# Optimization experiments

Hardware: AMD Instinct MI355X
Metric: run time of the kernel (lower is better)

## Reference

```python
import jax, jax.numpy as jnp
import numpy as np

TOPK_FRAC = 0.05
TOPK_MIN = 5
TOPK_MAX = 64


def setup_inputs() -> dict:
    key = jax.random.key(0)
    ks = jax.random.split(key, 8)
    N, H, B = 131072, 256, 512
    x = jax.random.normal(ks[0], (N, H), dtype=jnp.float32)
    batch = jnp.sort(jax.random.randint(ks[1], (N,), 0, B, dtype=jnp.int32))
    W1 = jax.random.normal(ks[2], (H, H // 2), dtype=jnp.float32) * 0.05
    b1 = jax.random.normal(ks[3], (H // 2,), dtype=jnp.float32) * 0.05
    W2 = jax.random.normal(ks[4], (H // 2, 1), dtype=jnp.float32) * 0.05
    b2 = jax.random.normal(ks[5], (1,), dtype=jnp.float32) * 0.05
    Wf = jax.random.normal(ks[6], (4 * H, H), dtype=jnp.float32) * 0.05
    bf = jax.random.normal(ks[7], (H,), dtype=jnp.float32) * 0.05
    return {"x": x, "batch": batch, "W1": W1, "b1": b1, "W2": W2,
            "b2": b2, "Wf": Wf, "bf": bf, "num_graphs": B}


def _forward(x, batch, W1, b1, W2, b2, Wf, bf, B):
    N = x.shape[0]
    # attention scores per node: MLP -> scalar
    s = (jax.nn.relu(x @ W1 + b1) @ W2 + b2)[:, 0]  # [N]
    # pyg_softmax: segment-wise stable softmax over nodes of each graph
    seg_max = jax.ops.segment_max(s, batch, num_segments=B)
    seg_max = jnp.where(jnp.isfinite(seg_max), seg_max, 0.0)  # guard empty segs
    e = jnp.exp(s - seg_max[batch])
    denom = jax.ops.segment_sum(e, batch, num_segments=B)
    w = e / denom[batch]                                    # [N]
    # pools
    x_attn = jax.ops.segment_sum(x * w[:, None], batch, num_segments=B)
    counts = jax.ops.segment_sum(jnp.ones((N,), jnp.int32), batch, num_segments=B)
    cnt_f = jnp.maximum(counts, 1).astype(x.dtype)
    x_mean = jax.ops.segment_sum(x, batch, num_segments=B) / cnt_f[:, None]
    x_max = jax.ops.segment_max(x, batch, num_segments=B)
    x_max = jnp.where(counts[:, None] > 0, x_max, 0.0)
    # per-graph dynamic k
    n = counts
    k = jnp.maximum(TOPK_MIN, jnp.ceil(TOPK_FRAC * n.astype(jnp.float32)).astype(jnp.int32))
    k = jnp.minimum(jnp.minimum(k, TOPK_MAX), n)            # [B]
    # fused segment top-k mean: sort nodes by (batch asc, w desc), keep rank<k
    order = jnp.lexsort((-w, batch))
    starts = jnp.concatenate([jnp.zeros((1,), jnp.int32), jnp.cumsum(counts)[:-1].astype(jnp.int32)])
    bs = batch[order]
    rank = jnp.arange(N, dtype=jnp.int32) - starts[bs]
    sel = (rank < k[bs]).astype(x.dtype)
    x_topk = jax.ops.segment_sum(x[order] * sel[:, None], bs, num_segments=B)
    x_topk = x_topk / jnp.maximum(k, 1).astype(x.dtype)[:, None]
    g = jax.nn.relu(jnp.concatenate([x_mean, x_attn, x_max, x_topk], axis=1) @ Wf + bf)
    return g


def reference(x, batch, W1, b1, W2, b2, Wf, bf, num_graphs):
    return _forward(x, batch, W1, b1, W2, b2, Wf, bf, num_graphs)
```

## Files before the change

### kernel.cpp

```cpp
#include <hip/hip_runtime.h>
#include <math.h>

#define H 256
#define HH 128
#define B_GRAPHS 512

typedef __attribute__((ext_vector_type(8))) short bfrag8;
typedef __attribute__((ext_vector_type(16))) float f32x16;

__global__ void k_prep_w1(const float* __restrict__ W1, ushort* __restrict__ W1b) {
  const int idx = blockIdx.x * 256 + threadIdx.x;
  const int k = idx >> 7, c = idx & 127;
  const float v = W1[idx];
  const uint u = __builtin_bit_cast(uint, v);
  const float r = v - __builtin_bit_cast(float, u & 0xFFFF0000u);
  const int base = (((k >> 4) * 2 + ((k >> 3) & 1)) * 128 + c) * 8 + (k & 7);
  W1b[base] = (ushort)(u >> 16);
  W1b[32768 + base] = (ushort)(__builtin_bit_cast(uint, r) >> 16);
}

__global__ void k_seg_bounds(const int* __restrict__ batch, int* __restrict__ seg_start,
                             int N, int B) {
  int b = blockIdx.x * blockDim.x + threadIdx.x;
  if (b > B) return;
  int lo = 0, hi = N;
  while (lo < hi) {
    int mid = (lo + hi) >> 1;
    if (batch[mid] < b) lo = mid + 1; else hi = mid;
  }
  seg_start[b] = lo;
}

__global__ __launch_bounds__(256, 4) void k_score_mfma(
    const float* __restrict__ x, const ushort* __restrict__ W1b,
    const float* __restrict__ b1, const float* __restrict__ W2,
    const float* __restrict__ b2, float* __restrict__ s_out) {
  __shared__ ushort ash[2][32][260];
  const int t = threadIdx.x;
  const int lane = t & 63;
  const int w = t >> 6;
  const int nl = lane & 31, g = lane >> 5;
  const int node0 = blockIdx.x * 32;

  {
    const float* base = x + (size_t)node0 * H + w * 2048 + lane * 4;
    float4 v[8];
#pragma unroll
    for (int i = 0; i < 8; ++i) v[i] = *(const float4*)(base + i * 256);
#pragma unroll
    for (int i = 0; i < 8; ++i) {
      const int r = w * 8 + i;
      const float vals[4] = {v[i].x, v[i].y, v[i].z, v[i].w};
      ushort m[4], rr[4];
#pragma unroll
      for (int e = 0; e < 4; ++e) {
        const uint u = __builtin_bit_cast(uint, vals[e]);
        m[e] = (ushort)(u >> 16);
        const float res = vals[e] - __builtin_bit_cast(float, u & 0xFFFF0000u);
        rr[e] = (ushort)(__builtin_bit_cast(uint, res) >> 16);
      }
      *(uint2*)&ash[0][r][lane * 4] =
          make_uint2((uint)m[0] | ((uint)m[1] << 16), (uint)m[2] | ((uint)m[3] << 16));
      *(uint2*)&ash[1][r][lane * 4] =
          make_uint2((uint)rr[0] | ((uint)rr[1] << 16), (uint)rr[2] | ((uint)rr[3] << 16));
    }
  }
  __syncthreads();

  f32x16 acc[2];
  acc[0] = (f32x16)0.f;
  acc[1] = (f32x16)0.f;
  const ushort* bbase = W1b + (size_t)(w * 32 + nl) * 8 + (size_t)g * 1024;

#pragma unroll
  for (int kks = 0; kks < 16; ++kks) {
    const bfrag8 a0 = *(const bfrag8*)&ash[0][nl][kks * 16 + g * 8];
    const bfrag8 a1 = *(const bfrag8*)&ash[1][nl][kks * 16 + g * 8];
    const bfrag8 b0 = *(const bfrag8*)(bbase + kks * 2048);
    const bfrag8 b1f = *(const bfrag8*)(bbase + kks * 2048 + 32768);
    acc[0] = __builtin_amdgcn_mfma_f32_32x32x16_bf16(a0, b0, acc[0], 0, 0, 0);
    acc[1] = __builtin_amdgcn_mfma_f32_32x32x16_bf16(a0, b1f, acc[1], 0, 0, 0);
    acc[0] = __builtin_amdgcn_mfma_f32_32x32x16_bf16(a1, b0, acc[0], 0, 0, 0);
  }

  __syncthreads();
  float* part = (float*)ash;
#pragma unroll
  for (int r = 0; r < 16; ++r) {
    const int row = (r & 3) + 8 * (r >> 2) + 4 * g;
    part[row * 132 + w * 32 + nl] = acc[0][r] + acc[1][r];
  }
  __syncthreads();
  {
    const int node = t >> 3, seg = t & 7;
    float v = 0.f;
#pragma unroll
    for (int e = 0; e < 16; ++e) {
      const int hcol = seg * 16 + e;
      const float hv = part[node * 132 + hcol] + b1[hcol];
      v = fmaf(fmaxf(hv, 0.f), W2[hcol], v);
    }
#pragma unroll
    for (int m = 1; m <= 4; m <<= 1) v += __shfl_xor(v, m);
    if ((t & 7) == 0) s_out[node0 + node] = v + b2[0];
  }
}

__global__ __launch_bounds__(512) void k_pool_fused(const float* __restrict__ x,
                                                    const float* __restrict__ s,
                                                    const int* __restrict__ seg_start,
                                                    float* __restrict__ pooled) {
  const int b = blockIdx.x;
  const int t = threadIdx.x;
  const int start = seg_start[b];
  const int end = seg_start[b + 1];
  const int n = end - start;

  __shared__ float s_lds[1024];
  __shared__ float red[512];
  __shared__ float thr_sh;
  __shared__ int thri_sh;
  __shared__ float r4[8][264];

  const bool fits = (n <= 1024);
  if (fits) {
    for (int i = t; i < n; i += 512) s_lds[i] = s[start + i];
  }
  __syncthreads();
  const float* sseg = fits ? s_lds : (s + start);

  float m = -INFINITY;
  for (int i = t; i < n; i += 512) m = fmaxf(m, sseg[i]);
  red[t] = m;
  __syncthreads();
  for (int off = 256; off > 0; off >>= 1) {
    if (t < off) red[t] = fmaxf(red[t], red[t + off]);
    __syncthreads();
  }
  const float smax = red[0];
  __syncthreads();
  float d = 0.f;
  for (int i = t; i < n; i += 512) d += __expf(sseg[i] - smax);
  red[t] = d;
  __syncthreads();
  for (int off = 256; off > 0; off >>= 1) {
    if (t < off) red[t] += red[t + off];
    __syncthreads();
  }
  const float denom = red[0];
  __syncthreads();
  const float inv_denom = (denom > 0.f) ? 1.f / denom : 0.f;

  int k = 0;
  if (n > 0) {
    k = (int)ceilf(0.05f * (float)n);
    if (k < 5) k = 5;
    if (k > 64) k = 64;
    if (k > n) k = n;
  }

  if (t < 64) {
    float pk = INFINITY;
    int pidx = -1;
    for (int r = 0; r < k; ++r) {
      float bk = -INFINITY;
      int bi = 0x7fffffff;
      for (int i = t; i < n; i += 64) {
        const float si = sseg[i];
        const int gi = start + i;
        const bool below = (si < pk) || (si == pk && gi > pidx);
        if (below && (si > bk || (si == bk && gi < bi))) { bk = si; bi = gi; }
      }
#pragma unroll
      for (int off = 32; off > 0; off >>= 1) {
        const float ok = __shfl_xor(bk, off);
        const int oi = __shfl_xor(bi, off);
        if (ok > bk || (ok == bk && oi < bi)) { bk = ok; bi = oi; }
      }
      pk = bk;
      pidx = bi;
    }
    if (t == 0) {
      thr_sh = (k > 0) ? pk : INFINITY;
      thri_sh = (k > 0) ? pidx : -1;
    }
  }
  __syncthreads();
  const float thr = thr_sh;
  const int thri = thri_sh;

  const int fq = t & 63;
  const int sub = t >> 6;
  float mean[4] = {0.f, 0.f, 0.f, 0.f};
  float attn[4] = {0.f, 0.f, 0.f, 0.f};
  float tk[4] = {0.f, 0.f, 0.f, 0.f};
  float mx[4] = {-INFINITY, -INFINITY, -INFINITY, -INFINITY};
  for (int i = sub; i < n; i += 8) {
    const float si = sseg[i];
    const float wi = __expf(si - smax);
    const int gi = start + i;
    const bool sel = (si > thr) || (si == thr && gi <= thri);
    const float4 xv = *reinterpret_cast<const float4*>(x + (size_t)gi * H + fq * 4);
    mean[0] += xv.x; mean[1] += xv.y; mean[2] += xv.z; mean[3] += xv.w;
    attn[0] = fmaf(xv.x, wi, attn[0]);
    attn[1] = fmaf(xv.y, wi, attn[1]);
    attn[2] = fmaf(xv.z, wi, attn[2]);
    attn[3] = fmaf(xv.w, wi, attn[3]);
    mx[0] = fmaxf(mx[0], xv.x);
    mx[1] = fmaxf(mx[1], xv.y);
    mx[2] = fmaxf(mx[2], xv.z);
    mx[3] = fmaxf(mx[3], xv.w);
    if (sel) {
      tk[0] += xv.x; tk[1] += xv.y; tk[2] += xv.z; tk[3] += xv.w;
    }
  }
  float* po = pooled + (size_t)b * 1024;
  const float invn = 1.f / (float)(n > 0 ? n : 1);
  const float invk = (k > 0) ? 1.f / (float)k : 0.f;
  *reinterpret_cast<float4*>(&r4[sub][fq * 4]) = make_float4(mean[0], mean[1], mean[2], mean[3]);
  __syncthreads();
  if (t < 256) {
    float tot = 0.f;
#pragma unroll
    for (int q = 0; q < 8; ++q) tot += r4[q][t];
    po[t] = tot * invn;
  }
  __syncthreads();
  *reinterpret_cast<float4*>(&r4[sub][fq * 4]) = make_float4(attn[0], attn[1], attn[2], attn[3]);
  __syncthreads();
  if (t < 256) {
    float tot = 0.f;
#pragma unroll
    for (int q = 0; q < 8; ++q) tot += r4[q][t];
    po[256 + t] = tot * inv_denom;
  }
  __syncthreads();
  *reinterpret_cast<float4*>(&r4[sub][fq * 4]) = make_float4(mx[0], mx[1], mx[2], mx[3]);
  __syncthreads();
  if (t < 256) {
    float tot = -INFINITY;
#pragma unroll
    for (int q = 0; q < 8; ++q) tot = fmaxf(tot, r4[q][t]);
    po[512 + t] = (n > 0) ? tot : 0.f;
  }
  __syncthreads();
  *reinterpret_cast<float4*>(&r4[sub][fq * 4]) = make_float4(tk[0], tk[1], tk[2], tk[3]);
  __syncthreads();
  if (t < 256) {
    float tot = 0.f;
#pragma unroll
    for (int q = 0; q < 8; ++q) tot += r4[q][t];
    po[768 + t] = tot * invk;
  }
}

__global__ __launch_bounds__(256) void k_gemm(const float* __restrict__ pooled,
                                              const float* __restrict__ Wf,
                                              float* __restrict__ gacc) {
  const int t = threadIdx.x;
  const int r0 = blockIdx.x * 8;
  const int kc0 = blockIdx.y * 128;
  __shared__ float ps[8][132];
  {
    const int r = t >> 5;
    const int c = (t & 31) << 2;
    *reinterpret_cast<float4*>(&ps[r][c]) =
        *reinterpret_cast<const float4*>(pooled + (size_t)(r0 + r) * 1024 + kc0 + c);
  }
  __syncthreads();
  float acc[8];
#pragma unroll
  for (int r = 0; r < 8; ++r) acc[r] = 0.f;
#pragma unroll 4
  for (int c = 0; c < 128; ++c) {
    const float wf = Wf[(size_t)(kc0 + c) * 256 + t];
#pragma unroll
    for (int r = 0; r < 8; ++r) acc[r] = fmaf(ps[r][c], wf, acc[r]);
  }
  float* go = gacc + ((size_t)blockIdx.y * B_GRAPHS + r0) * 256;
#pragma unroll
  for (int r = 0; r < 8; ++r) go[r * 256 + t] = acc[r];
}

__global__ __launch_bounds__(256) void k_out(const float* __restrict__ gacc,
                                             const float* __restrict__ bf,
                                             float* __restrict__ out) {
  const int i = blockIdx.x * 256 + threadIdx.x;
  float v = bf[i & 255];
#pragma unroll
  for (int ks = 0; ks < 8; ++ks) v += gacc[(size_t)ks * (B_GRAPHS * 256) + i];
  out[i] = fmaxf(v, 0.f);
}

extern "C" void kernel_launch(void* const* d_in, const int* in_sizes, int n_in,
                              void* d_out, int out_size, void* d_ws, size_t ws_size,
                              hipStream_t stream) {
  const float* x  = (const float*)d_in[0];
  const int* batch = (const int*)d_in[1];
  const float* W1 = (const float*)d_in[2];
  const float* b1 = (const float*)d_in[3];
  const float* W2 = (const float*)d_in[4];
  const float* b2 = (const float*)d_in[5];
  const float* Wf = (const float*)d_in[6];
  const float* bf = (const float*)d_in[7];
  const int N = in_sizes[1];
  const int B = B_GRAPHS;

  float* ws = (float*)d_ws;
  float* s = ws;
  int* seg_start = (int*)(ws + N);
  float* pooled = ws + N + 1024;
  float* gacc = pooled + (size_t)B * 1024;
  ushort* W1b = (ushort*)(gacc + (size_t)8 * B * 256);

  k_prep_w1<<<dim3(128), dim3(256), 0, stream>>>(W1, W1b);
  k_seg_bounds<<<dim3((B + 1 + 255) / 256), dim3(256), 0, stream>>>(batch, seg_start, N, B);
  k_score_mfma<<<dim3(N / 32), dim3(256), 0, stream>>>(x, W1b, b1, W2, b2, s);
  k_pool_fused<<<dim3(B), dim3(512), 0, stream>>>(x, s, seg_start, pooled);
  k_gemm<<<dim3(B / 8, 8), dim3(256), 0, stream>>>(pooled, Wf, gacc);
  k_out<<<dim3((B * 256) / 256), dim3(256), 0, stream>>>(gacc, bf, (float*)d_out);
}
```

Measured before the change: 112.6 us.

## Load MFMA A-fragments directly from global and merge prep kernels

The score kernel no longer stages x through a bf16-split shared-memory tile. Each lane now loads its own 8-float slice from global per k-step and splits it into hi/lo bf16 fragments in registers, which drops the staging pass and a barrier and shrinks LDS enough to raise launch bounds to 8 blocks per CU. The W1 conversion and segment-bounds kernels are merged into one launch to save launch overhead. The per-lane global loads are strided by row (each lane reads 32 bytes from a different 1 KB row), so coalescing is worse than the previous contiguous staging loads.

Result: slower. 146.5 us (+30.1%).

```diff
diff --git a/kernel.cpp b/kernel.cpp
--- a/kernel.cpp
+++ b/kernel.cpp
@@ -8,87 +8,75 @@
 typedef __attribute__((ext_vector_type(8))) short bfrag8;
 typedef __attribute__((ext_vector_type(16))) float f32x16;
 
-__global__ void k_prep_w1(const float* __restrict__ W1, ushort* __restrict__ W1b) {
-  const int idx = blockIdx.x * 256 + threadIdx.x;
-  const int k = idx >> 7, c = idx & 127;
-  const float v = W1[idx];
-  const uint u = __builtin_bit_cast(uint, v);
-  const float r = v - __builtin_bit_cast(float, u & 0xFFFF0000u);
-  const int base = (((k >> 4) * 2 + ((k >> 3) & 1)) * 128 + c) * 8 + (k & 7);
-  W1b[base] = (ushort)(u >> 16);
-  W1b[32768 + base] = (ushort)(__builtin_bit_cast(uint, r) >> 16);
-}
-
-__global__ void k_seg_bounds(const int* __restrict__ batch, int* __restrict__ seg_start,
-                             int N, int B) {
-  int b = blockIdx.x * blockDim.x + threadIdx.x;
-  if (b > B) return;
-  int lo = 0, hi = N;
-  while (lo < hi) {
-    int mid = (lo + hi) >> 1;
-    if (batch[mid] < b) lo = mid + 1; else hi = mid;
-  }
-  seg_start[b] = lo;
-}
-
-__global__ __launch_bounds__(256, 4) void k_score_mfma(
+__global__ void k_prep(const float* __restrict__ W1, ushort* __restrict__ W1b,
+                       const int* __restrict__ batch, int* __restrict__ seg_start,
+                       int N, int B) {
+  const int blk = blockIdx.x;
+  if (blk < 128) {
+    const int idx = blk * 256 + threadIdx.x;
+    const int k = idx >> 7, c = idx & 127;
+    const float v = W1[idx];
+    const uint u = __builtin_bit_cast(uint, v);
+    const float r = v - __builtin_bit_cast(float, u & 0xFFFF0000u);
+    const int base = (((k >> 4) * 2 + ((k >> 3) & 1)) * 128 + c) * 8 + (k & 7);
+    W1b[base] = (ushort)(u >> 16);
+    W1b[32768 + base] = (ushort)(__builtin_bit_cast(uint, r) >> 16);
+  } else {
+    const int b = (blk - 128) * 256 + threadIdx.x;
+    if (b > B) return;
+    int lo = 0, hi = N;
+    while (lo < hi) {
+      int mid = (lo + hi) >> 1;
+      if (batch[mid] < b) lo = mid + 1; else hi = mid;
+    }
+    seg_start[b] = lo;
+  }
+}
+
+__device__ __forceinline__ void splitbf(const float4 v0, const float4 v1,
+                                        bfrag8& a0, bfrag8& a1) {
+  const float vals[8] = {v0.x, v0.y, v0.z, v0.w, v1.x, v1.y, v1.z, v1.w};
+#pragma unroll
+  for (int e = 0; e < 8; ++e) {
+    const uint u = __builtin_bit_cast(uint, vals[e]);
+    a0[e] = (short)(u >> 16);
+    const float r = vals[e] - __builtin_bit_cast(float, u & 0xFFFF0000u);
+    a1[e] = (short)(__builtin_bit_cast(uint, r) >> 16);
+  }
+}
+
+__global__ __launch_bounds__(256, 8) void k_score_mfma(
     const float* __restrict__ x, const ushort* __restrict__ W1b,
     const float* __restrict__ b1, const float* __restrict__ W2,
     const float* __restrict__ b2, float* __restrict__ s_out) {
-  __shared__ ushort ash[2][32][260];
+  __shared__ float part[32 * 132];
   const int t = threadIdx.x;
   const int lane = t & 63;
   const int w = t >> 6;
   const int nl = lane & 31, g = lane >> 5;
   const int node0 = blockIdx.x * 32;
 
-  {
-    const float* base = x + (size_t)node0 * H + w * 2048 + lane * 4;
-    float4 v[8];
-#pragma unroll
-    for (int i = 0; i < 8; ++i) v[i] = *(const float4*)(base + i * 256);
-#pragma unroll
-    for (int i = 0; i < 8; ++i) {
-      const int r = w * 8 + i;
-      const float vals[4] = {v[i].x, v[i].y, v[i].z, v[i].w};
-      ushort m[4], rr[4];
-#pragma unroll
-      for (int e = 0; e < 4; ++e) {
-        const uint u = __builtin_bit_cast(uint, vals[e]);
-        m[e] = (ushort)(u >> 16);
-        const float res = vals[e] - __builtin_bit_cast(float, u & 0xFFFF0000u);
-        rr[e] = (ushort)(__builtin_bit_cast(uint, res) >> 16);
-      }
-      *(uint2*)&ash[0][r][lane * 4] =
-          make_uint2((uint)m[0] | ((uint)m[1] << 16), (uint)m[2] | ((uint)m[3] << 16));
-      *(uint2*)&ash[1][r][lane * 4] =
-          make_uint2((uint)rr[0] | ((uint)rr[1] << 16), (uint)rr[2] | ((uint)rr[3] << 16));
-    }
-  }
-  __syncthreads();
-
-  f32x16 acc[2];
-  acc[0] = (f32x16)0.f;
-  acc[1] = (f32x16)0.f;
-  const ushort* bbase = W1b + (size_t)(w * 32 + nl) * 8 + (size_t)g * 1024;
-
+  const float* gsrc = x + (size_t)(node0 + nl) * H + g * 8;
+  const ushort* bbase = W1b + ((size_t)g * 128 + w * 32 + nl) * 8;
+
+  f32x16 acc0 = (f32x16)0.f, acc1 = (f32x16)0.f;
 #pragma unroll
   for (int kks = 0; kks < 16; ++kks) {
-    const bfrag8 a0 = *(const bfrag8*)&ash[0][nl][kks * 16 + g * 8];
-    const bfrag8 a1 = *(const bfrag8*)&ash[1][nl][kks * 16 + g * 8];
-    const bfrag8 b0 = *(const bfrag8*)(bbase + kks * 2048);
-    const bfrag8 b1f = *(const bfrag8*)(bbase + kks * 2048 + 32768);
-    acc[0] = __builtin_amdgcn_mfma_f32_32x32x16_bf16(a0, b0, acc[0], 0, 0, 0);
-    acc[1] = __builtin_amdgcn_mfma_f32_32x32x16_bf16(a0, b1f, acc[1], 0, 0, 0);
-    acc[0] = __builtin_amdgcn_mfma_f32_32x32x16_bf16(a1, b0, acc[0], 0, 0, 0);
-  }
-
-  __syncthreads();
-  float* part = (float*)ash;
+    const float4 v0 = *(const float4*)(gsrc + kks * 16);
+    const float4 v1 = *(const float4*)(gsrc + kks * 16 + 4);
+    bfrag8 a0, a1;
+    splitbf(v0, v1, a0, a1);
+    const bfrag8 b0 = *(const bfrag8*)(bbase + (size_t)kks * 2048);
+    const bfrag8 b1f = *(const bfrag8*)(bbase + (size_t)kks * 2048 + 32768);
+    acc0 = __builtin_amdgcn_mfma_f32_32x32x16_bf16(a0, b0, acc0, 0, 0, 0);
+    acc1 = __builtin_amdgcn_mfma_f32_32x32x16_bf16(a0, b1f, acc1, 0, 0, 0);
+    acc0 = __builtin_amdgcn_mfma_f32_32x32x16_bf16(a1, b0, acc0, 0, 0, 0);
+  }
+
 #pragma unroll
   for (int r = 0; r < 16; ++r) {
     const int row = (r & 3) + 8 * (r >> 2) + 4 * g;
-    part[row * 132 + w * 32 + nl] = acc[0][r] + acc[1][r];
+    part[row * 132 + w * 32 + nl] = acc0[r] + acc1[r];
   }
   __syncthreads();
   {
@@ -313,8 +301,7 @@
   float* gacc = pooled + (size_t)B * 1024;
   ushort* W1b = (ushort*)(gacc + (size_t)8 * B * 256);
 
-  k_prep_w1<<<dim3(128), dim3(256), 0, stream>>>(W1, W1b);
-  k_seg_bounds<<<dim3((B + 1 + 255) / 256), dim3(256), 0, stream>>>(batch, seg_start, N, B);
+  k_prep<<<dim3(131), dim3(256), 0, stream>>>(W1, W1b, batch, seg_start, N, B);
   k_score_mfma<<<dim3(N / 32), dim3(256), 0, stream>>>(x, W1b, b1, W2, b2, s);
   k_pool_fused<<<dim3(B), dim3(512), 0, stream>>>(x, s, seg_start, pooled);
   k_gemm<<<dim3(B / 8, 8), dim3(256), 0, stream>>>(pooled, Wf, gacc);
```
